# Kernel optimization log

Hardware: AMD Instinct MI355X
Metric: run time of the kernel (lower is better)

Reference implementation:

```python
import jax, jax.numpy as jnp
import numpy as np

N, E, D_IN, H, M, C, B = 50000, 800000, 256, 128, 64, 4, 128
NH, HD = 8, H // 8


def setup_inputs() -> dict:
    key = jax.random.key(0)
    ks = jax.random.split(key, 24)
    s = 0.05
    rn = lambda k, shp: (jax.random.normal(k, shp) * s).astype(jnp.float32)
    return {
        "x": jax.random.normal(ks[0], (N, D_IN), dtype=jnp.float32),
        "edge_index": jax.random.randint(ks[1], (2, E), 0, N),
        "batch": jnp.sort(jax.random.randint(ks[2], (N,), 0, B)),
        # feature_transform: Linear(D_IN->H) + LayerNorm(H)
        "w1": rn(ks[3], (D_IN, H)), "b1": jnp.zeros((H,), jnp.float32),
        "ln_g": jnp.ones((H,), jnp.float32), "ln_b": jnp.zeros((H,), jnp.float32),
        # 3 GCNConv(H->H) layers
        "gw1": rn(ks[4], (H, H)), "gb1": jnp.zeros((H,), jnp.float32),
        "gw2": rn(ks[5], (H, H)), "gb2": jnp.zeros((H,), jnp.float32),
        "gw3": rn(ks[6], (H, H)), "gb3": jnp.zeros((H,), jnp.float32),
        # memory bank + MultiheadAttention(H, 8 heads), torch layout (out,in)
        "memory_bank": jax.random.normal(ks[7], (M, H), dtype=jnp.float32),
        "in_proj_w": rn(ks[8], (3 * H, H)), "in_proj_b": jnp.zeros((3 * H,), jnp.float32),
        "out_w": rn(ks[9], (H, H)), "out_b": jnp.zeros((H,), jnp.float32),
        # classifier: Linear(2H->H) -> ReLU -> Linear(H->C)
        "cw1": rn(ks[10], (2 * H, H)), "cb1": jnp.zeros((H,), jnp.float32),
        "cw2": rn(ks[11], (H, C)), "cb2": jnp.zeros((C,), jnp.float32),
    }


def _layer_norm(x, g, b, eps=1e-5):
    mu = jnp.mean(x, axis=-1, keepdims=True)
    var = jnp.var(x, axis=-1, keepdims=True)
    return (x - mu) * jax.lax.rsqrt(var + eps) * g + b


def _gcn(x, W, b, row, col, norm):
    # PyG GCNConv: x' = D^-1/2 (A+I) D^-1/2 (x W) + b, aggregated at col (target)
    xw = x @ W
    msg = xw[row] * norm[:, None]                      # [E+N, H]
    out = jax.ops.segment_sum(msg, col, num_segments=N)
    return out + b


def reference(x, edge_index, batch, w1, b1, ln_g, ln_b, gw1, gb1, gw2, gb2, gw3, gb3,
              memory_bank, in_proj_w, in_proj_b, out_w, out_b, cw1, cb1, cw2, cb2):
    # feature transform (dropout is identity in eval)
    h = _layer_norm(jax.nn.relu(x @ w1 + b1), ln_g, ln_b)

    # GCN normalization with self-loops
    sl = jnp.arange(N)
    row = jnp.concatenate([edge_index[0], sl])
    col = jnp.concatenate([edge_index[1], sl])
    deg = jax.ops.segment_sum(jnp.ones_like(col, dtype=h.dtype), col, num_segments=N)
    dis = jax.lax.rsqrt(deg)                           # deg >= 1 from self-loops
    norm = dis[row] * dis[col]

    for W, b in ((gw1, gb1), (gw2, gb2), (gw3, gb3)):
        h = jax.nn.relu(_gcn(h, W, b, row, col, norm))

    # global mean pool per graph
    sums = jax.ops.segment_sum(h, batch, num_segments=B)
    cnts = jax.ops.segment_sum(jnp.ones((N,), h.dtype), batch, num_segments=B)
    pooled = sums / jnp.maximum(cnts, 1.0)[:, None]    # [B, H]

    # memory attention: query = pooled (len 1), kv = memory bank (shared)
    q = pooled @ in_proj_w[:H].T + in_proj_b[:H]       # [B, H]
    k = memory_bank @ in_proj_w[H:2 * H].T + in_proj_b[H:2 * H]  # [M, H]
    v = memory_bank @ in_proj_w[2 * H:].T + in_proj_b[2 * H:]    # [M, H]
    qh = q.reshape(B, NH, HD)
    kh = k.reshape(M, NH, HD)
    vh = v.reshape(M, NH, HD)
    scores = jnp.einsum('bhd,mhd->bhm', qh, kh) / jnp.sqrt(jnp.float32(HD))
    p = jax.nn.softmax(scores, axis=-1)
    attn = jnp.einsum('bhm,mhd->bhd', p, vh).reshape(B, H)
    mem = attn @ out_w.T + out_b                       # [B, H]

    # classifier on [pooled, memory_enhanced]
    z = jnp.concatenate([pooled, mem], axis=-1)        # [B, 2H]
    z = jax.nn.relu(z @ cw1 + cb1)
    return z @ cw2 + cb2                               # [B, C]
```

## Files before the change

kernel.cpp:

```cpp
#include <hip/hip_runtime.h>

#define NN 50000
#define EE 800000
#define DIN 256
#define H 128
#define MM 64
#define CC 4
#define BB 128
#define NHEAD 8
#define HDIM 16

#define NRW 50
#define RNODES 1000
#define NSB 625
#define ESL 1280

typedef _Float16 f16x8 __attribute__((ext_vector_type(8)));
typedef _Float16 f16x4 __attribute__((ext_vector_type(4)));
typedef float f32x4 __attribute__((ext_vector_type(4)));


__launch_bounds__(256)
__global__ void ecount(const int* __restrict__ col, int* __restrict__ bcnt) {
    __shared__ int hist[NRW];
    int b = blockIdx.x, t = threadIdx.x;
    if (t < NRW) hist[t] = 0;
    __syncthreads();
    int e0 = b * ESL;
    #pragma unroll
    for (int i = 0; i < ESL / 256; i++) {
        int c = col[e0 + t + i * 256];
        atomicAdd(&hist[c / RNODES], 1);
    }
    __syncthreads();
    if (t < NRW) bcnt[t * NSB + b] = hist[t];
}

__launch_bounds__(256)
__global__ void erange_tot(const int* __restrict__ bcnt, int* __restrict__ rtot) {
    __shared__ int red[4];
    int r = blockIdx.x, t = threadIdx.x;
    int s = 0;
    for (int b = t; b < NSB; b += 256) s += bcnt[r * NSB + b];
    #pragma unroll
    for (int m = 1; m < 64; m <<= 1) s += __shfl_xor(s, m, 64);
    if ((t & 63) == 0) red[t >> 6] = s;
    __syncthreads();
    if (t == 0) rtot[r] = red[0] + red[1] + red[2] + red[3];
}

__global__ void rscan(const int* __restrict__ rtot, int* __restrict__ rbase) {
    if (threadIdx.x == 0 && blockIdx.x == 0) {
        int run = 0;
        for (int i = 0; i < NRW; i++) { rbase[i] = run; run += rtot[i]; }
    }
}

__launch_bounds__(256)
__global__ void esbase(const int* __restrict__ bcnt, const int* __restrict__ rbase,
                       int* __restrict__ sbase) {
    __shared__ int sb[256];
    __shared__ int carry;
    int r = blockIdx.x, t = threadIdx.x;
    if (t == 0) carry = rbase[r];
    __syncthreads();
    for (int base = 0; base < NSB; base += 256) {
        int b = base + t;
        int v = (b < NSB) ? bcnt[r * NSB + b] : 0;
        sb[t] = v;
        __syncthreads();
        for (int off = 1; off < 256; off <<= 1) {
            int x = (t >= off) ? sb[t - off] : 0;
            __syncthreads();
            sb[t] += x;
            __syncthreads();
        }
        if (b < NSB) sbase[r * NSB + b] = carry + sb[t] - v;
        __syncthreads();
        if (t == 255) carry += sb[255];
        __syncthreads();
    }
}

__launch_bounds__(256)
__global__ void escatter(const int* __restrict__ row, const int* __restrict__ col,
                         const int* __restrict__ sbase, int2* __restrict__ ebuf) {
    __shared__ int cur[NRW];
    int b = blockIdx.x, t = threadIdx.x;
    if (t < NRW) cur[t] = sbase[t * NSB + b];
    __syncthreads();
    int e0 = b * ESL;
    #pragma unroll
    for (int i = 0; i < ESL / 256; i++) {
        int e = e0 + t + i * 256;
        int c = col[e];
        int u = row[e];
        int r = c / RNODES;
        int p = atomicAdd(&cur[r], 1);
        ebuf[p] = make_int2(u, c - r * RNODES);
    }
}

__launch_bounds__(512)
__global__ void csr_build(const int2* __restrict__ ebuf, const int* __restrict__ rbase,
                          int* __restrict__ degcnt, int* __restrict__ offs,
                          float* __restrict__ dis, int* __restrict__ csr) {
    __shared__ int hist[RNODES];
    __shared__ int cur[RNODES];
    __shared__ int sb[512];
    int r = blockIdx.x, t = threadIdx.x;
    int r0 = r * RNODES;
    int rb = rbase[r];
    int re = (r + 1 < NRW) ? rbase[r + 1] : EE;
    for (int i = t; i < RNODES; i += 512) hist[i] = 0;
    __syncthreads();
    for (int e = rb + t; e < re; e += 512) atomicAdd(&hist[ebuf[e].y], 1);
    __syncthreads();
    int i0 = 2 * t, i1 = 2 * t + 1;
    int d0 = (i0 < RNODES) ? hist[i0] : 0;
    int d1 = (i1 < RNODES) ? hist[i1] : 0;
    int ps = d0 + d1;
    sb[t] = ps;
    __syncthreads();
    for (int off = 1; off < 512; off <<= 1) {
        int x = (t >= off) ? sb[t - off] : 0;
        __syncthreads();
        sb[t] += x;
        __syncthreads();
    }
    int excl = sb[t] - ps;
    if (i0 < RNODES) {
        cur[i0] = excl;
        degcnt[r0 + i0] = d0;
        offs[r0 + i0] = rb + excl;
        dis[r0 + i0] = rsqrtf((float)(d0 + 1));
    }
    if (i1 < RNODES) {
        cur[i1] = excl + d0;
        degcnt[r0 + i1] = d1;
        offs[r0 + i1] = rb + excl + d0;
        dis[r0 + i1] = rsqrtf((float)(d1 + 1));
    }
    __syncthreads();
    for (int e = rb + t; e < re; e += 512) {
        int2 ed = ebuf[e];
        int p = atomicAdd(&cur[ed.y], 1);
        csr[rb + p] = ed.x;
    }
}


__global__ void graph_bounds(const int* __restrict__ batch, int* __restrict__ gstart) {
    int v = blockIdx.x * blockDim.x + threadIdx.x;
    if (v >= NN) return;
    int b = batch[v];
    if (v == 0) {
        for (int g = 0; g <= b; g++) gstart[g] = 0;
    } else {
        int pb = batch[v - 1];
        for (int g = pb + 1; g <= b; g++) gstart[g] = v;
    }
    if (v == NN - 1) {
        for (int g = b + 1; g <= BB; g++) gstart[g] = NN;
    }
}


__global__ void wsplit_all(const float* __restrict__ w1, const float* __restrict__ gw1,
                           const float* __restrict__ gw2, const float* __restrict__ gw3,
                           _Float16* __restrict__ wf1, _Float16* __restrict__ wfg1,
                           _Float16* __restrict__ wfg2, _Float16* __restrict__ wfg3) {
    int b = blockIdx.x;
    int l = threadIdx.x;
    const float* Wg; _Float16* outw; int KT, f;
    if (b < 64)       { Wg = w1;  outw = wf1;  KT = 8; f = b; }
    else if (b < 96)  { Wg = gw1; outw = wfg1; KT = 4; f = b - 64; }
    else if (b < 128) { Wg = gw2; outw = wfg2; KT = 4; f = b - 96; }
    else              { Wg = gw3; outw = wfg3; KT = 4; f = b - 128; }
    int kt = f >> 3, ct = f & 7;
    int k0 = kt * 32 + (l >> 4) * 8;
    int c = ct * 16 + (l & 15);
    f16x8 hi, lo;
    #pragma unroll
    for (int j = 0; j < 8; j++) {
        float w = Wg[(size_t)(k0 + j) * H + c];
        _Float16 hh = (_Float16)w;
        hi[j] = hh;
        lo[j] = (_Float16)(w - (float)hh);
    }
    *reinterpret_cast<f16x8*>(outw + ((size_t)f * 64 + l) * 8) = hi;
    *reinterpret_cast<f16x8*>(outw + ((size_t)KT * 8 * 64 * 8) + ((size_t)f * 64 + l) * 8) = lo;
}


template <int K, bool LN, int OMODE, bool POOL, int AIN>
__launch_bounds__(256)
__global__ void mfma_linear(const void* __restrict__ Ap, const _Float16* __restrict__ Wf,
                            const float* __restrict__ bias,
                            const float* __restrict__ ln_g, const float* __restrict__ ln_b,
                            const float* __restrict__ dis, const int* __restrict__ batch,
                            void* __restrict__ outp) {
    constexpr int KT = K / 32;
    __shared__ __align__(16) _Float16 stage[2][8192];
    int t = threadIdx.x;
    int wv = t >> 6, l = t & 63;
    int lm = l & 15, lg = l >> 4;
    int rowBase = blockIdx.x * 64;
    int arow = rowBase + wv * 16 + lm;
    int arc = min(arow, NN - 1);
    const float* A32 = (const float*)Ap;
    const _Float16* A16 = (const _Float16*)Ap;
    const f16x8* __restrict__ BhG = reinterpret_cast<const f16x8*>(Wf);
    const f16x8* __restrict__ BlG = BhG + KT * 8 * 64;

    auto stage_kt = [&](int b, int kt) {
        f16x8* dstH = reinterpret_cast<f16x8*>(&stage[b][0]);
        f16x8* dstL = reinterpret_cast<f16x8*>(&stage[b][4096]);
        int wo = wv * 128 + l;
        #pragma unroll
        for (int i = 0; i < 2; i++) {
            int o = wo + i * 64;
            dstH[o] = BhG[(size_t)kt * 512 + o];
            dstL[o] = BlG[(size_t)kt * 512 + o];
        }
    };

    float4 aAll[16]; f16x8 aAll16[8];
    if constexpr (AIN == 0) {
        #pragma unroll
        for (int kt = 0; kt < KT; kt++) {
            const float* ap = A32 + (size_t)arc * K + kt * 32 + lg * 8;
            aAll[2 * kt]     = *(const float4*)ap;
            aAll[2 * kt + 1] = *(const float4*)(ap + 4);
        }
    } else {
        #pragma unroll
        for (int kt = 0; kt < KT; kt++)
            aAll16[kt] = *(const f16x8*)(A16 + (size_t)arc * K + kt * 32 + lg * 8);
    }

    f32x4 acc[8];
    #pragma unroll
    for (int ct = 0; ct < 8; ct++) acc[ct] = (f32x4){0.f, 0.f, 0.f, 0.f};

    stage_kt(0, 0);
    __syncthreads();
    int buf = 0;
    #pragma unroll
    for (int kt = 0; kt < KT; kt++) {
        if (kt + 1 < KT) stage_kt(buf ^ 1, kt + 1);
        f16x8 ah, al;
        if constexpr (AIN == 0) {
            float4 a0c = aAll[2 * kt], a1c = aAll[2 * kt + 1];
            float av[8] = {a0c.x, a0c.y, a0c.z, a0c.w, a1c.x, a1c.y, a1c.z, a1c.w};
            #pragma unroll
            for (int j = 0; j < 8; j++) {
                _Float16 hh = (_Float16)av[j];
                ah[j] = hh;
                al[j] = (_Float16)(av[j] - (float)hh);
            }
        } else {
            ah = aAll16[kt];
        }
        #pragma unroll
        for (int ct = 0; ct < 8; ct++) {
            f16x8 bh = *reinterpret_cast<const f16x8*>(&stage[buf][(ct * 64 + l) * 8]);
            f16x8 bl = *reinterpret_cast<const f16x8*>(&stage[buf][4096 + (ct * 64 + l) * 8]);
            acc[ct] = __builtin_amdgcn_mfma_f32_16x16x32_f16(ah, bh, acc[ct], 0, 0, 0);
            acc[ct] = __builtin_amdgcn_mfma_f32_16x16x32_f16(ah, bl, acc[ct], 0, 0, 0);
            if constexpr (AIN == 0)
                acc[ct] = __builtin_amdgcn_mfma_f32_16x16x32_f16(al, bh, acc[ct], 0, 0, 0);
        }
        __syncthreads();
        buf ^= 1;
    }

    float bv[8], gv[8], lbv[8];
    #pragma unroll
    for (int ct = 0; ct < 8; ct++) {
        int c = ct * 16 + lm;
        bv[ct] = bias[c];
        if constexpr (LN) { gv[ct] = ln_g[c]; lbv[ct] = ln_b[c]; }
    }

    float vals[4][8];
    #pragma unroll
    for (int q = 0; q < 4; q++) {
        float s = 0.f, sq = 0.f;
        #pragma unroll
        for (int ct = 0; ct < 8; ct++) {
            float v = fmaxf(acc[ct][q] + bv[ct], 0.f);
            vals[q][ct] = v;
            s += v; sq += v * v;
        }
        if constexpr (LN) {
            #pragma unroll
            for (int m = 1; m < 16; m <<= 1) {
                s  += __shfl_xor(s,  m, 64);
                sq += __shfl_xor(sq, m, 64);
            }
            float mean = s * (1.f / 128.f);
            float var  = sq * (1.f / 128.f) - mean * mean;
            float inv  = rsqrtf(var + 1e-5f);
            #pragma unroll
            for (int ct = 0; ct < 8; ct++)
                vals[q][ct] = (vals[q][ct] - mean) * inv * gv[ct] + lbv[ct];
        }
    }

    if constexpr (POOL) {
        __shared__ float tile[64][129];
        __shared__ int bl64[64];
        float* psums = (float*)outp;
        #pragma unroll
        for (int q = 0; q < 4; q++) {
            int r64 = wv * 16 + lg * 4 + q;
            #pragma unroll
            for (int ct = 0; ct < 8; ct++)
                tile[r64][ct * 16 + lm] = vals[q][ct];
        }
        if (t < 64) bl64[t] = batch[min(rowBase + t, NN - 1)];
        __syncthreads();
        if (t < H) {
            float pacc = 0.f;
            int curb = bl64[0];
            int rmax = min(64, NN - rowBase);
            for (int r = 0; r < rmax; r++) {
                int b = bl64[r];
                if (b != curb) {
                    atomicAdd(&psums[curb * H + t], pacc);
                    pacc = 0.f; curb = b;
                }
                pacc += tile[r][t];
            }
            atomicAdd(&psums[curb * H + t], pacc);
        }
    } else {
        #pragma unroll
        for (int q = 0; q < 4; q++) {
            int rr = rowBase + wv * 16 + lg * 4 + q;
            if (rr < NN) {
                if constexpr (OMODE == 1) {
                    _Float16* o16 = (_Float16*)outp;
                    float sc = dis[rr];
                    #pragma unroll
                    for (int ct = 0; ct < 8; ct++)
                        o16[(size_t)rr * H + ct * 16 + lm] = (_Float16)(vals[q][ct] * sc);
                } else {
                    float* o32 = (float*)outp;
                    #pragma unroll
                    for (int ct = 0; ct < 8; ct++)
                        o32[(size_t)rr * H + ct * 16 + lm] = vals[q][ct];
                }
            }
        }
    }
}


__launch_bounds__(256)
__global__ void agg_kernel(const _Float16* __restrict__ g16, const int* __restrict__ offs,
                           const int* __restrict__ degcnt, const int* __restrict__ csr,
                           const float* __restrict__ dis, _Float16* __restrict__ out16) {
    __shared__ int idx[8][64];
    int grp = threadIdx.x >> 5;
    int l = threadIdx.x & 31;
    int v = blockIdx.x * 8 + grp;
    int beg = offs[v], cnt = degcnt[v];
    idx[grp][l]      = (l      < cnt) ? csr[beg + l]      : v;
    idx[grp][l + 32] = (l + 32 < cnt) ? csr[beg + l + 32] : v;

    const f16x4* __restrict__ G = reinterpret_cast<const f16x4*>(g16);
    float dv = dis[v];
    f16x4 gvh = G[(size_t)v * 32 + l];
    float4 gv = make_float4((float)gvh[0], (float)gvh[1], (float)gvh[2], (float)gvh[3]);
    float4 acc = gv;
    int n0 = min(cnt, 64);
    int m0 = (n0 + 7) & ~7;

    for (int i = 0; i < m0; i += 8) {
        f16x4 tv[8];
        #pragma unroll
        for (int jj = 0; jj < 8; jj++)
            tv[jj] = G[(size_t)idx[grp][i + jj] * 32 + l];
        #pragma unroll
        for (int jj = 0; jj < 8; jj++) {
            acc.x += (float)tv[jj][0];
            acc.y += (float)tv[jj][1];
            acc.z += (float)tv[jj][2];
            acc.w += (float)tv[jj][3];
        }
    }
    float pad = (float)(m0 - n0);
    acc.x -= pad * gv.x; acc.y -= pad * gv.y;
    acc.z -= pad * gv.z; acc.w -= pad * gv.w;

    for (int i = 64; i < cnt; i++) {
        f16x4 a = G[(size_t)csr[beg + i] * 32 + l];
        acc.x += (float)a[0]; acc.y += (float)a[1];
        acc.z += (float)a[2]; acc.w += (float)a[3];
    }
    f16x4 o;
    o[0] = (_Float16)(dv * acc.x); o[1] = (_Float16)(dv * acc.y);
    o[2] = (_Float16)(dv * acc.z); o[3] = (_Float16)(dv * acc.w);
    reinterpret_cast<f16x4*>(out16)[(size_t)v * 32 + l] = o;
}


__global__ void kv_kernel(const float* __restrict__ mb, const float* __restrict__ ipw,
                          const float* __restrict__ ipb,
                          float* __restrict__ kbuf, float* __restrict__ vbuf) {
    __shared__ float rowv[H];
    int m = blockIdx.x, i = threadIdx.x;
    rowv[i] = mb[m * H + i];
    __syncthreads();
    float ak = 0.f, av = 0.f;
    for (int j = 0; j < H; j++) {
        float x = rowv[j];
        ak = fmaf(x, ipw[(size_t)(H + i) * H + j], ak);
        av = fmaf(x, ipw[(size_t)(2 * H + i) * H + j], av);
    }
    kbuf[m * H + i] = ak + ipb[H + i];
    vbuf[m * H + i] = av + ipb[2 * H + i];
}


__launch_bounds__(128)
__global__ void attn_kernel(const float* __restrict__ psums, const int* __restrict__ gstart,
                            const float* __restrict__ kbuf, const float* __restrict__ vbuf,
                            const float* __restrict__ ipw, const float* __restrict__ ipb,
                            const float* __restrict__ out_w, const float* __restrict__ out_b,
                            const float* __restrict__ cw1, const float* __restrict__ cb1,
                            const float* __restrict__ cw2, const float* __restrict__ cb2,
                            float* __restrict__ out) {
    __shared__ float pooled[H], q[H], attn[H], z[2 * H], c1[H], sc[NHEAD * MM];
    int b = blockIdx.x, t = threadIdx.x;
    float cn = (float)max(gstart[b + 1] - gstart[b], 1);
    float pv = psums[b * H + t] / cn;
    pooled[t] = pv;
    z[t] = pv;
    __syncthreads();
    float a = 0.f;
    for (int j = 0; j < H; j++) a = fmaf(pooled[j], ipw[(size_t)t * H + j], a);
    q[t] = a + ipb[t];
    __syncthreads();
    for (int sidx = t; sidx < NHEAD * MM; sidx += 128) {
        int hh = sidx >> 6, m = sidx & 63;
        float s2 = 0.f;
        for (int d = 0; d < HDIM; d++)
            s2 = fmaf(q[hh * HDIM + d], kbuf[m * H + hh * HDIM + d], s2);
        sc[sidx] = s2 * 0.25f;
    }
    __syncthreads();
    if (t < NHEAD) {
        float mx = -1e30f;
        for (int m = 0; m < MM; m++) mx = fmaxf(mx, sc[t * MM + m]);
        float ssum = 0.f;
        for (int m = 0; m < MM; m++) { float e = expf(sc[t * MM + m] - mx); sc[t * MM + m] = e; ssum += e; }
        float inv = 1.f / ssum;
        for (int m = 0; m < MM; m++) sc[t * MM + m] *= inv;
    }
    __syncthreads();
    {
        int hh = t >> 4;
        float a2 = 0.f;
        for (int m = 0; m < MM; m++) a2 = fmaf(sc[hh * MM + m], vbuf[m * H + t], a2);
        attn[t] = a2;
    }
    __syncthreads();
    float mm = 0.f;
    for (int j = 0; j < H; j++) mm = fmaf(attn[j], out_w[(size_t)t * H + j], mm);
    z[H + t] = mm + out_b[t];
    __syncthreads();
    float cc = 0.f;
    for (int j = 0; j < 2 * H; j++) cc = fmaf(z[j], cw1[(size_t)j * H + t], cc);
    c1[t] = fmaxf(cc + cb1[t], 0.f);
    __syncthreads();
    if (t < CC) {
        float o = 0.f;
        for (int j = 0; j < H; j++) o = fmaf(c1[j], cw2[j * CC + t], o);
        out[b * CC + t] = o + cb2[t];
    }
}


extern "C" void kernel_launch(void* const* d_in, const int* in_sizes, int n_in,
                              void* d_out, int out_size, void* d_ws, size_t ws_size,
                              hipStream_t stream) {
    const float* x      = (const float*)d_in[0];
    const int*   eidx   = (const int*)d_in[1];
    const int*   batch  = (const int*)d_in[2];
    const float* w1     = (const float*)d_in[3];
    const float* b1     = (const float*)d_in[4];
    const float* ln_g   = (const float*)d_in[5];
    const float* ln_b   = (const float*)d_in[6];
    const float* gw1    = (const float*)d_in[7];
    const float* gb1    = (const float*)d_in[8];
    const float* gw2    = (const float*)d_in[9];
    const float* gb2    = (const float*)d_in[10];
    const float* gw3    = (const float*)d_in[11];
    const float* gb3    = (const float*)d_in[12];
    const float* memb   = (const float*)d_in[13];
    const float* ipw    = (const float*)d_in[14];
    const float* ipb    = (const float*)d_in[15];
    const float* out_w  = (const float*)d_in[16];
    const float* out_b  = (const float*)d_in[17];
    const float* cw1    = (const float*)d_in[18];
    const float* cb1    = (const float*)d_in[19];
    const float* cw2    = (const float*)d_in[20];
    const float* cb2    = (const float*)d_in[21];

    const int* row = eidx;
    const int* col = eidx + EE;

    char* ws = (char*)d_ws;
    size_t off = 0;
    auto alloc = [&](size_t bytes) -> void* {
        void* p = ws + off;
        off += (bytes + 255) & ~(size_t)255;
        return p;
    };
    _Float16* a16 = (_Float16*)alloc((size_t)NN * H * 2);
    _Float16* g16 = (_Float16*)alloc((size_t)NN * H * 2);
    char*  zbeg   = ws + off;
    float* psums  = (float*)alloc((size_t)BB * H * 4);
    size_t zbytes = (size_t)((ws + off) - zbeg);
    int*   degcnt = (int*)alloc((size_t)NN * 4);
    float* dis    = (float*)alloc((size_t)NN * 4);
    int*   offs   = (int*)alloc((size_t)NN * 4);
    int*   csr    = (int*)alloc((size_t)EE * 4);
    int2*  ebuf   = (int2*)alloc((size_t)EE * 8);
    int*   bcnt   = (int*)alloc((size_t)NRW * NSB * 4);
    int*   sbase  = (int*)alloc((size_t)NRW * NSB * 4);
    int*   rtot   = (int*)alloc(256);
    int*   rbase  = (int*)alloc(256);
    int*   gstart = (int*)alloc((size_t)(BB + 1) * 4);
    float* kbuf   = (float*)alloc((size_t)MM * H * 4);
    float* vbuf   = (float*)alloc((size_t)MM * H * 4);
    _Float16* wf1 = (_Float16*)alloc((size_t)2 * DIN * H * 2);
    _Float16* wfg1 = (_Float16*)alloc((size_t)2 * H * H * 2);
    _Float16* wfg2 = (_Float16*)alloc((size_t)2 * H * H * 2);
    _Float16* wfg3 = (_Float16*)alloc((size_t)2 * H * H * 2);
    (void)ws_size; (void)in_sizes; (void)n_in; (void)out_size;

    hipMemsetAsync(zbeg, 0, zbytes, stream);

    ecount<<<NSB, 256, 0, stream>>>(col, bcnt);
    erange_tot<<<NRW, 256, 0, stream>>>(bcnt, rtot);
    rscan<<<1, 64, 0, stream>>>(rtot, rbase);
    esbase<<<NRW, 256, 0, stream>>>(bcnt, rbase, sbase);
    escatter<<<NSB, 256, 0, stream>>>(row, col, sbase, ebuf);
    csr_build<<<NRW, 512, 0, stream>>>(ebuf, rbase, degcnt, offs, dis, csr);

    graph_bounds<<<(NN + 255) / 256, 256, 0, stream>>>(batch, gstart);

    wsplit_all<<<160, 64, 0, stream>>>(w1, gw1, gw2, gw3, wf1, wfg1, wfg2, wfg3);

    const int LGRID = (NN + 63) / 64;
    const int AGRID = NN / 8;

    mfma_linear<DIN, true, 1, false, 0><<<LGRID, 256, 0, stream>>>(x, wf1, b1, ln_g, ln_b, dis, nullptr, g16);

    agg_kernel<<<AGRID, 256, 0, stream>>>(g16, offs, degcnt, csr, dis, a16);
    mfma_linear<H, false, 1, false, 1><<<LGRID, 256, 0, stream>>>(a16, wfg1, gb1, nullptr, nullptr, dis, nullptr, g16);
    agg_kernel<<<AGRID, 256, 0, stream>>>(g16, offs, degcnt, csr, dis, a16);
    mfma_linear<H, false, 1, false, 1><<<LGRID, 256, 0, stream>>>(a16, wfg2, gb2, nullptr, nullptr, dis, nullptr, g16);
    agg_kernel<<<AGRID, 256, 0, stream>>>(g16, offs, degcnt, csr, dis, a16);
    mfma_linear<H, false, 0, true, 1><<<LGRID, 256, 0, stream>>>(a16, wfg3, gb3, nullptr, nullptr, dis, batch, psums);

    kv_kernel<<<MM, H, 0, stream>>>(memb, ipw, ipb, kbuf, vbuf);
    attn_kernel<<<BB, H, 0, stream>>>(psums, gstart, kbuf, vbuf, ipw, ipb, out_w, out_b,
                                      cw1, cb1, cw2, cb2, (float*)d_out);
}
```

Measured before the change: 235.9 us.

## Split edge buffer into row/col arrays, widen csr_build, fold memset

The packed int2 edge buffer is replaced by a separate int row array and a 16-bit local-column array, which shrinks the bytes read in the histogram pass of csr_build. csr_build moves from 512 to 1024 threads per block, so each thread handles one node in the scan. The psums zeroing memset is folded into graph_bounds to drop one API call. In exchange the 1024-thread scan adds more barrier steps, and csr_build still runs on only 50 blocks.

```diff
diff --git a/kernel.cpp b/kernel.cpp
--- a/kernel.cpp
+++ b/kernel.cpp
@@ -84,7 +84,8 @@
 
 __launch_bounds__(256)
 __global__ void escatter(const int* __restrict__ row, const int* __restrict__ col,
-                         const int* __restrict__ sbase, int2* __restrict__ ebuf) {
+                         const int* __restrict__ sbase, int* __restrict__ erow,
+                         unsigned short* __restrict__ ecol) {
     __shared__ int cur[NRW];
     int b = blockIdx.x, t = threadIdx.x;
     if (t < NRW) cur[t] = sbase[t * NSB + b];
@@ -97,61 +98,55 @@
         int u = row[e];
         int r = c / RNODES;
         int p = atomicAdd(&cur[r], 1);
-        ebuf[p] = make_int2(u, c - r * RNODES);
-    }
-}
-
-__launch_bounds__(512)
-__global__ void csr_build(const int2* __restrict__ ebuf, const int* __restrict__ rbase,
+        erow[p] = u;
+        ecol[p] = (unsigned short)(c - r * RNODES);
+    }
+}
+
+__launch_bounds__(1024)
+__global__ void csr_build(const int* __restrict__ erow, const unsigned short* __restrict__ ecol,
+                          const int* __restrict__ rbase,
                           int* __restrict__ degcnt, int* __restrict__ offs,
                           float* __restrict__ dis, int* __restrict__ csr) {
     __shared__ int hist[RNODES];
     __shared__ int cur[RNODES];
-    __shared__ int sb[512];
+    __shared__ int sb[1024];
     int r = blockIdx.x, t = threadIdx.x;
     int r0 = r * RNODES;
     int rb = rbase[r];
     int re = (r + 1 < NRW) ? rbase[r + 1] : EE;
-    for (int i = t; i < RNODES; i += 512) hist[i] = 0;
-    __syncthreads();
-    for (int e = rb + t; e < re; e += 512) atomicAdd(&hist[ebuf[e].y], 1);
-    __syncthreads();
-    int i0 = 2 * t, i1 = 2 * t + 1;
-    int d0 = (i0 < RNODES) ? hist[i0] : 0;
-    int d1 = (i1 < RNODES) ? hist[i1] : 0;
-    int ps = d0 + d1;
-    sb[t] = ps;
-    __syncthreads();
-    for (int off = 1; off < 512; off <<= 1) {
+    if (t < RNODES) hist[t] = 0;
+    __syncthreads();
+    for (int e = rb + t; e < re; e += 1024) atomicAdd(&hist[ecol[e]], 1);
+    __syncthreads();
+    int d = (t < RNODES) ? hist[t] : 0;
+    sb[t] = d;
+    __syncthreads();
+    for (int off = 1; off < 1024; off <<= 1) {
         int x = (t >= off) ? sb[t - off] : 0;
         __syncthreads();
         sb[t] += x;
         __syncthreads();
     }
-    int excl = sb[t] - ps;
-    if (i0 < RNODES) {
-        cur[i0] = excl;
-        degcnt[r0 + i0] = d0;
-        offs[r0 + i0] = rb + excl;
-        dis[r0 + i0] = rsqrtf((float)(d0 + 1));
-    }
-    if (i1 < RNODES) {
-        cur[i1] = excl + d0;
-        degcnt[r0 + i1] = d1;
-        offs[r0 + i1] = rb + excl + d0;
-        dis[r0 + i1] = rsqrtf((float)(d1 + 1));
-    }
-    __syncthreads();
-    for (int e = rb + t; e < re; e += 512) {
-        int2 ed = ebuf[e];
-        int p = atomicAdd(&cur[ed.y], 1);
-        csr[rb + p] = ed.x;
-    }
-}
-
-
-__global__ void graph_bounds(const int* __restrict__ batch, int* __restrict__ gstart) {
+    int excl = sb[t] - d;
+    if (t < RNODES) {
+        cur[t] = excl;
+        degcnt[r0 + t] = d;
+        offs[r0 + t] = rb + excl;
+        dis[r0 + t] = rsqrtf((float)(d + 1));
+    }
+    __syncthreads();
+    for (int e = rb + t; e < re; e += 1024) {
+        int p = atomicAdd(&cur[ecol[e]], 1);
+        csr[rb + p] = erow[e];
+    }
+}
+
+
+__global__ void graph_bounds(const int* __restrict__ batch, int* __restrict__ gstart,
+                             float* __restrict__ psums) {
     int v = blockIdx.x * blockDim.x + threadIdx.x;
+    if (v < BB * H) psums[v] = 0.f;
     if (v >= NN) return;
     int b = batch[v];
     if (v == 0) {
@@ -522,14 +517,13 @@
     };
     _Float16* a16 = (_Float16*)alloc((size_t)NN * H * 2);
     _Float16* g16 = (_Float16*)alloc((size_t)NN * H * 2);
-    char*  zbeg   = ws + off;
     float* psums  = (float*)alloc((size_t)BB * H * 4);
-    size_t zbytes = (size_t)((ws + off) - zbeg);
     int*   degcnt = (int*)alloc((size_t)NN * 4);
     float* dis    = (float*)alloc((size_t)NN * 4);
     int*   offs   = (int*)alloc((size_t)NN * 4);
     int*   csr    = (int*)alloc((size_t)EE * 4);
-    int2*  ebuf   = (int2*)alloc((size_t)EE * 8);
+    int*   erow   = (int*)alloc((size_t)EE * 4);
+    unsigned short* ecol = (unsigned short*)alloc((size_t)EE * 2);
     int*   bcnt   = (int*)alloc((size_t)NRW * NSB * 4);
     int*   sbase  = (int*)alloc((size_t)NRW * NSB * 4);
     int*   rtot   = (int*)alloc(256);
@@ -543,16 +537,14 @@
     _Float16* wfg3 = (_Float16*)alloc((size_t)2 * H * H * 2);
     (void)ws_size; (void)in_sizes; (void)n_in; (void)out_size;
 
-    hipMemsetAsync(zbeg, 0, zbytes, stream);
-
     ecount<<<NSB, 256, 0, stream>>>(col, bcnt);
     erange_tot<<<NRW, 256, 0, stream>>>(bcnt, rtot);
     rscan<<<1, 64, 0, stream>>>(rtot, rbase);
     esbase<<<NRW, 256, 0, stream>>>(bcnt, rbase, sbase);
-    escatter<<<NSB, 256, 0, stream>>>(row, col, sbase, ebuf);
-    csr_build<<<NRW, 512, 0, stream>>>(ebuf, rbase, degcnt, offs, dis, csr);
-
-    graph_bounds<<<(NN + 255) / 256, 256, 0, stream>>>(batch, gstart);
+    escatter<<<NSB, 256, 0, stream>>>(row, col, sbase, erow, ecol);
+    csr_build<<<NRW, 1024, 0, stream>>>(erow, ecol, rbase, degcnt, offs, dis, csr);
+
+    graph_bounds<<<(NN + 255) / 256, 256, 0, stream>>>(batch, gstart, psums);
 
     wsplit_all<<<160, 64, 0, stream>>>(w1, gw1, gw2, gw3, wf1, wfg1, wfg2, wfg3);
 
```

New measurement: 234.6 us. Within noise of the previous version (-0.6%).
